# Kernel optimization log

Hardware: AMD Instinct MI355X
Metric: run time of the kernel (lower is better)

The kernel has to match this reference:

```python
import jax, jax.numpy as jnp
import numpy as np

N, E, G = 65536, 262144, 2048
DIN, H, F, L, P, TASK = 9, 300, 32, 5, 3, 1
DG = H + F + 1024 + 167  # 1523


def setup_inputs() -> dict:
    key = jax.random.key(0)
    ks = jax.random.split(key, 24)
    s = 0.02
    inp = {
        'x': jax.random.normal(ks[0], (N, DIN), jnp.float32),
        'morgan': jax.random.uniform(ks[1], (G, 1024), jnp.float32),
        'maccs': jax.random.uniform(ks[2], (G, 167), jnp.float32),
        'edge_index': jax.random.randint(ks[3], (2, E), 0, N, jnp.int32),
        'batch': jnp.sort(jax.random.randint(ks[4], (N,), 0, G, jnp.int32)),
        # node feature encoder
        'W_emb': s * jax.random.normal(ks[5], (DIN, H), jnp.float32),
        'b_emb': jnp.zeros((H,), jnp.float32),
        # GIN conv MLPs (L layers): H -> 2H -> H
        'gin_W1': s * jax.random.normal(ks[6], (L, H, 2 * H), jnp.float32),
        'gin_b1': jnp.zeros((L, 2 * H), jnp.float32),
        'gin_W2': s * jax.random.normal(ks[7], (L, 2 * H, H), jnp.float32),
        'gin_b2': jnp.zeros((L, H), jnp.float32),
        'bn_scale': jnp.ones((L, H), jnp.float32),
        'bn_bias': jnp.zeros((L, H), jnp.float32),
        'eps': jnp.zeros((L,), jnp.float32),
        # virtual node: init embedding + update MLPs (L-1 layers)
        'vn0': jnp.zeros((H,), jnp.float32),
        'vn_W1': s * jax.random.normal(ks[8], (L - 1, H, 2 * H), jnp.float32),
        'vn_b1': jnp.zeros((L - 1, 2 * H), jnp.float32),
        'vn_W2': s * jax.random.normal(ks[9], (L - 1, 2 * H, H), jnp.float32),
        'vn_b2': jnp.zeros((L - 1, H), jnp.float32),
        # predictor MLP: DG -> 2H -> TASK
        'Wp1': s * jax.random.normal(ks[10], (DG, 2 * H), jnp.float32),
        'bp1': jnp.zeros((2 * H,), jnp.float32),
        'Wp2': s * jax.random.normal(ks[11], (2 * H, TASK), jnp.float32),
        'bp2': jnp.zeros((TASK,), jnp.float32),
    }
    return inp


def _seg_mean(v, seg, n):
    s = jax.ops.segment_sum(v, seg, num_segments=n)
    c = jax.ops.segment_sum(jnp.ones((v.shape[0], 1), v.dtype), seg, num_segments=n)
    return s / jnp.maximum(c, 1.0)


def _bn(z, scale, bias):
    m = z.mean(0)
    v = z.var(0)
    return (z - m) * jax.lax.rsqrt(v + 1e-5) * scale + bias


def _gnn_and_predict(x, morgan, maccs, W_emb, b_emb, gin_W1, gin_b1, gin_W2, gin_b2,
                     bn_scale, bn_bias, eps, vn0, vn_W1, vn_b1, vn_W2, vn_b2,
                     Wp1, bp1, Wp2, bp2, edge_index, batch):
    n = x.shape[0]
    g = morgan.shape[0]
    nl = gin_W1.shape[0]
    src, dst = edge_index[0], edge_index[1]

    # GIN-virtual backbone (eval mode, dropout off). Note: GNN input is the
    # original x (the permuted ids are appended AFTER the GNN), so h is
    # permutation-independent and computed once.
    h = x @ W_emb + b_emb
    vn = jnp.broadcast_to(vn0, (g, vn0.shape[0]))
    for l in range(nl):
        hv = h + vn[batch]                                       # [N,H]
        agg = jax.ops.segment_sum(hv[src], dst, num_segments=n)  # neighbor sum
        z = (1.0 + eps[l]) * hv + agg
        z = jax.nn.relu(z @ gin_W1[l] + gin_b1[l]) @ gin_W2[l] + gin_b2[l]
        z = _bn(z, bn_scale[l], bn_bias[l])
        if l < nl - 1:
            z = jax.nn.relu(z)
        h = h + z  # residual
        if l < nl - 1:  # virtual node update
            vt = jax.ops.segment_sum(hv, batch, num_segments=g) + vn
            vn = vn + jax.nn.relu(jax.nn.relu(vt @ vn_W1[l] + vn_b1[l]) @ vn_W2[l] + vn_b2[l])

    pooled_h = _seg_mean(h, batch, g)  # [G,H]

    # Segmented random permutation of tiled eye(F) ids, averaged over P perms.
    # Each node gets one_hot(perm_rank_within_graph % F); rank computed by a
    # single lexsort over (batch, random) instead of a per-graph Python loop.
    counts = jax.ops.segment_sum(jnp.ones((n,), jnp.int32), batch, num_segments=g)
    starts = jnp.concatenate([jnp.zeros((1,), jnp.int32),
                              jnp.cumsum(counts)[:-1].astype(jnp.int32)])
    pkey = jax.random.key(42)
    acc = jnp.zeros((g, F), h.dtype)
    for p in range(P):
        r = jax.random.uniform(jax.random.fold_in(pkey, p), (n,))
        order = jnp.lexsort((r, batch))                       # sort by graph, then random
        local = jnp.arange(n, dtype=jnp.int32) - starts[batch[order]]
        rank = jnp.zeros((n,), jnp.int32).at[order].set(local)  # random rank in graph
        ids = jax.nn.one_hot(rank % F, F, dtype=h.dtype)        # [N,F]
        acc = acc + _seg_mean(ids, batch, g)
    id_pool = acc / P

    # h_rep order matches torch: [pooled h | pooled ids | morgan | maccs]
    h_rep = jnp.concatenate([pooled_h, id_pool, morgan, maccs], axis=1)  # [G,1523]
    return jax.nn.relu(h_rep @ Wp1 + bp1) @ Wp2 + bp2  # [G,TASK]


def reference(x, morgan, maccs, W_emb, b_emb, gin_W1, gin_b1, gin_W2, gin_b2,
              bn_scale, bn_bias, eps, vn0, vn_W1, vn_b1, vn_W2, vn_b2,
              Wp1, bp1, Wp2, bp2, edge_index, batch):
    return _gnn_and_predict(x, morgan, maccs, W_emb, b_emb, gin_W1, gin_b1,
                            gin_W2, gin_b2, bn_scale, bn_bias, eps, vn0,
                            vn_W1, vn_b1, vn_W2, vn_b2, Wp1, bp1, Wp2, bp2,
                            edge_index, batch)
```

## Files before the change

kernel.cpp:

```cpp
#include <hip/hip_runtime.h>

typedef unsigned short u16;
typedef unsigned int u32;
typedef __attribute__((ext_vector_type(8))) short bf16x8_t;
typedef __attribute__((ext_vector_type(4))) float f32x4_t;

#define kN 65536
#define kE 262144
#define kG 2048
#define kH 300
#define kH2 600
#define kL 5
#define kF 32
#define kDG 1523
#define KP_H 320
#define KP_H2 640
#define KP_DG 1536
#define NP_H2 640
#define NP_H 320
#define HVS 320
#define HVS32 160

__device__ __forceinline__ float bf2f(u16 x) {
    union { u32 u; float f; } v; v.u = ((u32)x) << 16; return v.f;
}
__device__ __forceinline__ u16 f2bf(float f) {
    union { float f; u32 u; } v; v.f = f;
    u32 u = v.u;
    u32 r = (u + 0x7fffu + ((u >> 16) & 1u)) >> 16;
    return (u16)r;
}
__device__ __forceinline__ float blo(u32 v) { return bf2f((u16)(v & 0xffffu)); }
__device__ __forceinline__ float bhi(u32 v) { return bf2f((u16)(v >> 16)); }
__device__ __forceinline__ u32 pack2(float lo, float hi) {
    return (u32)f2bf(lo) | ((u32)f2bf(hi) << 16);
}

__device__ __forceinline__ void gld16(const u16* g, u16* l) {
    __builtin_amdgcn_global_load_lds(
        (const __attribute__((address_space(1))) u32*)g,
        (__attribute__((address_space(3))) u32*)l, 16, 0, 0);
}

__device__ __forceinline__ void swz_tile(int& m, int& n) {
    int p = blockIdx.x + gridDim.x * blockIdx.y;
    int xcd = p & 7;
    int q = p >> 3;
    int NB = gridDim.y;
    int mb8 = gridDim.x >> 3;
    m = xcd * mb8 + q / NB;
    n = q % NB;
}

__global__ void transpose_k(const float* __restrict__ W, u16* __restrict__ Wt,
                            int K, int NN, int NP, int KP, long total) {
    long idx = (long)blockIdx.x * 256 + threadIdx.x;
    if (idx >= total) return;
    int per = NP * KP;
    int b = (int)(idx / per);
    int r = (int)(idx % per);
    int n = r / KP;
    int k = r % KP;
    u16 v = 0;
    if (n < NN && k < K) v = f2bf(W[(long)b * K * NN + (long)k * NN + n]);
    Wt[idx] = v;
}

__global__ void hist_g_k(const int* __restrict__ batch, int* __restrict__ counts) {
    int n = blockIdx.x * 256 + threadIdx.x;
    if (n < kN) atomicAdd(&counts[batch[n]], 1);
}

__global__ void scan_g_k(const int* __restrict__ counts, int* __restrict__ starts) {
    __shared__ int s[1024];
    int t = threadIdx.x;
    int c0 = counts[2 * t], c1 = counts[2 * t + 1];
    s[t] = c0 + c1;
    __syncthreads();
    for (int off = 1; off < 1024; off <<= 1) {
        int v = (t >= off) ? s[t - off] : 0;
        __syncthreads();
        s[t] += v;
        __syncthreads();
    }
    int excl = (t > 0) ? s[t - 1] : 0;
    starts[2 * t] = excl;
    starts[2 * t + 1] = excl + c0;
}

__global__ void hist_n_k(const int* __restrict__ ei, int* __restrict__ cnt) {
    int e = blockIdx.x * 256 + threadIdx.x;
    if (e < kE) atomicAdd(&cnt[ei[kE + e]], 1);
}

__global__ void scanA_k(const int* __restrict__ cnt, int* __restrict__ start, int* __restrict__ bsum) {
    __shared__ int s[1024];
    int b = blockIdx.x, t = threadIdx.x;
    int v = cnt[b * 1024 + t];
    s[t] = v;
    __syncthreads();
    for (int off = 1; off < 1024; off <<= 1) {
        int u = (t >= off) ? s[t - off] : 0;
        __syncthreads();
        s[t] += u;
        __syncthreads();
    }
    start[b * 1024 + t] = s[t] - v;
    if (t == 1023) bsum[b] = s[1023];
}

__global__ void scanB_k(int* __restrict__ bsum) {
    if (threadIdx.x == 0) {
        int s = 0;
        for (int i = 0; i < kN / 1024; i++) { s += bsum[i]; bsum[i] = s; }
    }
}

__global__ void scanC_k(int* __restrict__ start, const int* __restrict__ bsum) {
    int b = blockIdx.x, t = threadIdx.x;
    int add = (b > 0) ? bsum[b - 1] : 0;
    start[b * 1024 + t] += add;
    if (b == kN / 1024 - 1 && t == 1023) start[kN] = bsum[kN / 1024 - 1];
}

__global__ void fill_n_k(const int* __restrict__ ei, const int* __restrict__ start,
                         int* __restrict__ fill, int* __restrict__ perm) {
    int e = blockIdx.x * 256 + threadIdx.x;
    if (e >= kE) return;
    int s = ei[e], d = ei[kE + e];
    int pos = start[d] + atomicAdd(&fill[d], 1);
    perm[pos] = s;
}

__global__ __launch_bounds__(256) void embed_k(
    const float* __restrict__ x, const float* __restrict__ W,
    const float* __restrict__ b, const float* __restrict__ vn0,
    u32* __restrict__ hv32) {
    __shared__ float sW[9 * kH];
    __shared__ float sBV[kH];
    int tid = threadIdx.x;
    for (int i = tid; i < 9 * kH; i += 256) sW[i] = W[i];
    for (int i = tid; i < kH; i += 256) sBV[i] = b[i] + vn0[i];
    __syncthreads();
    int wave = tid >> 6, lane = tid & 63;
    int n = blockIdx.x * 4 + wave;
    float xv[9];
    #pragma unroll
    for (int d = 0; d < 9; d++) xv[d] = x[n * 9 + d];
    #pragma unroll
    for (int p = 0; p < 3; p++) {
        int ii = lane + p * 64;
        if (ii < 150) {
            int c0 = 2 * ii;
            float a0 = sBV[c0], a1 = sBV[c0 + 1];
            #pragma unroll
            for (int d = 0; d < 9; d++) {
                a0 += xv[d] * sW[d * kH + c0];
                a1 += xv[d] * sW[d * kH + c0 + 1];
            }
            hv32[(long)n * HVS32 + ii] = pack2(a0, a1);
        } else if (ii < HVS32) {
            hv32[(long)n * HVS32 + ii] = 0u;
        }
    }
}

__global__ void vninit_k(const float* __restrict__ vn0, float* __restrict__ vn) {
    int g = blockIdx.x, c = threadIdx.x;
    if (c < kH) vn[g * kH + c] = vn0[c];
}

__global__ __launch_bounds__(256) void gather_combine_k(
    const u32* __restrict__ hv32, const int* __restrict__ start_n,
    const int* __restrict__ perm, const float* __restrict__ eps, int l,
    u32* __restrict__ out32, float* __restrict__ stats) {
    int tid = threadIdx.x;
    int wave = tid >> 6, lane = tid & 63;
    int n = blockIdx.x * 4 + wave;
    int st = start_n[n], en = start_n[n + 1];
    int i0 = lane, i1 = lane + 64, i2 = lane + 128;
    bool p2 = (i2 < 150);
    float a0 = 0.f, b0 = 0.f, a1 = 0.f, b1 = 0.f, a2 = 0.f, b2 = 0.f;
    int e = st;
    for (; e + 4 <= en; e += 4) {
        const u32* rA = hv32 + (long)perm[e] * HVS32;
        const u32* rB = hv32 + (long)perm[e + 1] * HVS32;
        const u32* rC = hv32 + (long)perm[e + 2] * HVS32;
        const u32* rD = hv32 + (long)perm[e + 3] * HVS32;
        u32 vA0 = rA[i0], vA1 = rA[i1], vA2 = p2 ? rA[i2] : 0u;
        u32 vB0 = rB[i0], vB1 = rB[i1], vB2 = p2 ? rB[i2] : 0u;
        u32 vC0 = rC[i0], vC1 = rC[i1], vC2 = p2 ? rC[i2] : 0u;
        u32 vD0 = rD[i0], vD1 = rD[i1], vD2 = p2 ? rD[i2] : 0u;
        a0 += (blo(vA0) + blo(vB0)) + (blo(vC0) + blo(vD0));
        b0 += (bhi(vA0) + bhi(vB0)) + (bhi(vC0) + bhi(vD0));
        a1 += (blo(vA1) + blo(vB1)) + (blo(vC1) + blo(vD1));
        b1 += (bhi(vA1) + bhi(vB1)) + (bhi(vC1) + bhi(vD1));
        a2 += (blo(vA2) + blo(vB2)) + (blo(vC2) + blo(vD2));
        b2 += (bhi(vA2) + bhi(vB2)) + (bhi(vC2) + bhi(vD2));
    }
    for (; e + 2 <= en; e += 2) {
        const u32* rA = hv32 + (long)perm[e] * HVS32;
        const u32* rB = hv32 + (long)perm[e + 1] * HVS32;
        u32 vA0 = rA[i0], vA1 = rA[i1], vA2 = p2 ? rA[i2] : 0u;
        u32 vB0 = rB[i0], vB1 = rB[i1], vB2 = p2 ? rB[i2] : 0u;
        a0 += blo(vA0) + blo(vB0); b0 += bhi(vA0) + bhi(vB0);
        a1 += blo(vA1) + blo(vB1); b1 += bhi(vA1) + bhi(vB1);
        a2 += blo(vA2) + blo(vB2); b2 += bhi(vA2) + bhi(vB2);
    }
    if (e < en) {
        const u32* rA = hv32 + (long)perm[e] * HVS32;
        u32 vA0 = rA[i0], vA1 = rA[i1], vA2 = p2 ? rA[i2] : 0u;
        a0 += blo(vA0); b0 += bhi(vA0);
        a1 += blo(vA1); b1 += bhi(vA1);
        a2 += blo(vA2); b2 += bhi(vA2);
    }
    const u32* self = hv32 + (long)n * HVS32;
    float ep = 1.f + eps[l];
    u32 s0 = self[i0], s1 = self[i1];
    u32* o = out32 + (long)n * HVS32;
    o[i0] = pack2(ep * blo(s0) + a0, ep * bhi(s0) + b0);
    o[i1] = pack2(ep * blo(s1) + a1, ep * bhi(s1) + b1);
    if (p2) {
        u32 s2 = self[i2];
        o[i2] = pack2(ep * blo(s2) + a2, ep * bhi(s2) + b2);
    } else if (i2 < HVS32) {
        o[i2] = 0u;
    }
    int gz = blockIdx.x * 256 + tid;
    if (gz < 2 * kH) stats[gz] = 0.f;
}

__global__ __launch_bounds__(256) void vt_fin_k(
    const u32* __restrict__ hv32, const float* __restrict__ vncur,
    const int* __restrict__ counts, const int* __restrict__ starts,
    u32* __restrict__ vt32) {
    int tid = threadIdx.x, wave = tid >> 6, lane = tid & 63;
    int g = blockIdx.x * 4 + wave;
    int cnt = counts[g], st = starts[g];
    int i0 = lane, i1 = lane + 64, i2 = lane + 128;
    bool p2 = (i2 < 150);
    float a0 = 0.f, b0 = 0.f, a1 = 0.f, b1 = 0.f, a2 = 0.f, b2 = 0.f;
    int i = 0;
    for (; i + 4 <= cnt; i += 4) {
        const u32* rA = hv32 + (long)(st + i) * HVS32;
        const u32* rB = hv32 + (long)(st + i + 1) * HVS32;
        const u32* rC = hv32 + (long)(st + i + 2) * HVS32;
        const u32* rD = hv32 + (long)(st + i + 3) * HVS32;
        u32 vA0 = rA[i0], vA1 = rA[i1], vA2 = p2 ? rA[i2] : 0u;
        u32 vB0 = rB[i0], vB1 = rB[i1], vB2 = p2 ? rB[i2] : 0u;
        u32 vC0 = rC[i0], vC1 = rC[i1], vC2 = p2 ? rC[i2] : 0u;
        u32 vD0 = rD[i0], vD1 = rD[i1], vD2 = p2 ? rD[i2] : 0u;
        a0 += (blo(vA0) + blo(vB0)) + (blo(vC0) + blo(vD0));
        b0 += (bhi(vA0) + bhi(vB0)) + (bhi(vC0) + bhi(vD0));
        a1 += (blo(vA1) + blo(vB1)) + (blo(vC1) + blo(vD1));
        b1 += (bhi(vA1) + bhi(vB1)) + (bhi(vC1) + bhi(vD1));
        a2 += (blo(vA2) + blo(vB2)) + (blo(vC2) + blo(vD2));
        b2 += (bhi(vA2) + bhi(vB2)) + (bhi(vC2) + bhi(vD2));
    }
    for (; i < cnt; i++) {
        const u32* rA = hv32 + (long)(st + i) * HVS32;
        u32 vA0 = rA[i0], vA1 = rA[i1], vA2 = p2 ? rA[i2] : 0u;
        a0 += blo(vA0); b0 += bhi(vA0);
        a1 += blo(vA1); b1 += bhi(vA1);
        a2 += blo(vA2); b2 += bhi(vA2);
    }
    const float* vg = vncur + g * kH;
    vt32[(long)g * HVS32 + i0] = pack2(a0 + vg[2 * i0], b0 + vg[2 * i0 + 1]);
    vt32[(long)g * HVS32 + i1] = pack2(a1 + vg[2 * i1], b1 + vg[2 * i1 + 1]);
    if (p2) vt32[(long)g * HVS32 + i2] = pack2(a2 + vg[2 * i2], b2 + vg[2 * i2 + 1]);
    else if (i2 < HVS32) vt32[(long)g * HVS32 + i2] = 0u;
}

template<int ACT, int OUT_BF16, int BN_STATS>
__global__ __launch_bounds__(256) void gemm_k(
    const u16* __restrict__ A, const u16* __restrict__ Wt,
    const float* __restrict__ bias, void* __restrict__ out,
    float* __restrict__ stats,
    int KP, int NN, int out_stride, int store_cols) {
    __shared__ __align__(16) u16 lA[128 * 64];
    __shared__ __align__(16) u16 lB[128 * 64];
    __shared__ float sred[128][2];

    const int tid = threadIdx.x;
    const int lane = tid & 63;
    const int wave = tid >> 6;
    const int l16 = lane & 15;
    const int quad = lane >> 4;
    const int wm = (wave & 1) * 64;
    const int wn = (wave >> 1) * 64;
    int sm, sn;
    swz_tile(sm, sn);
    const long tm = (long)sm * 128;
    const int tn = sn * 128;

    const int srow = lane >> 3;
    const int sch = (lane & 7) ^ srow;

    f32x4_t acc[4][4];
    #pragma unroll
    for (int i = 0; i < 4; i++)
        #pragma unroll
        for (int j = 0; j < 4; j++) acc[i][j] = (f32x4_t){0.f, 0.f, 0.f, 0.f};

    for (int k0 = 0; k0 < KP; k0 += 64) {
        __syncthreads();
        #pragma unroll
        for (int j = 0; j < 4; j++) {
            int rb = wave * 32 + j * 8;
            int r = rb + srow;
            gld16(A + (tm + r) * KP + k0 + sch * 8, &lA[rb * 64]);
            gld16(Wt + (long)(tn + r) * KP + k0 + sch * 8, &lB[rb * 64]);
        }
        __syncthreads();
        #pragma unroll
        for (int ks = 0; ks < 2; ks++) {
            bf16x8_t af[4], bfr[4];
            #pragma unroll
            for (int mt = 0; mt < 4; mt++) {
                int row = wm + mt * 16 + l16;
                int phys = (ks * 4 + quad) ^ (l16 & 7);
                af[mt] = *(const bf16x8_t*)&lA[row * 64 + phys * 8];
            }
            #pragma unroll
            for (int nt = 0; nt < 4; nt++) {
                int row = wn + nt * 16 + l16;
                int phys = (ks * 4 + quad) ^ (l16 & 7);
                bfr[nt] = *(const bf16x8_t*)&lB[row * 64 + phys * 8];
            }
            #pragma unroll
            for (int mt = 0; mt < 4; mt++)
                #pragma unroll
                for (int nt = 0; nt < 4; nt++)
                    acc[mt][nt] = __builtin_amdgcn_mfma_f32_16x16x32_bf16(af[mt], bfr[nt], acc[mt][nt], 0, 0, 0);
        }
    }

    if (BN_STATS) {
        if (tid < 128) { sred[tid][0] = 0.f; sred[tid][1] = 0.f; }
    }
    __syncthreads();

    #pragma unroll
    for (int nt = 0; nt < 4; nt++) {
        int col = tn + wn + nt * 16 + l16;
        float bv = (col < NN) ? bias[col] : 0.f;
        float s = 0.f, s2 = 0.f;
        #pragma unroll
        for (int mt = 0; mt < 4; mt++) {
            #pragma unroll
            for (int r = 0; r < 4; r++) {
                long row = tm + wm + mt * 16 + quad * 4 + r;
                float v = acc[mt][nt][r] + bv;
                if (ACT) v = fmaxf(v, 0.f);
                float sv = (col < NN) ? v : 0.f;
                if (col < store_cols) {
                    if (OUT_BF16) ((u16*)out)[row * out_stride + col] = f2bf(sv);
                    else          ((float*)out)[row * out_stride + col] = sv;
                }
                s += sv; s2 += sv * sv;
            }
        }
        if (BN_STATS) {
            atomicAdd(&sred[wn + nt * 16 + l16][0], s);
            atomicAdd(&sred[wn + nt * 16 + l16][1], s2);
        }
    }
    if (BN_STATS) {
        __syncthreads();
        if (tid < 128) {
            int col = tn + tid;
            if (col < NN) {
                atomicAdd(&stats[col], sred[tid][0]);
                atomicAdd(&stats[NN + col], sred[tid][1]);
            }
        }
    }
}

template<int ACT, int OUT_MODE, int BN_STATS>
__global__ __launch_bounds__(256) void gemm64_k(
    const u16* __restrict__ A, const u16* __restrict__ Wt,
    const float* __restrict__ bias, void* __restrict__ out,
    float* __restrict__ stats, const float* __restrict__ vnacc,
    int KP, int NN, int out_stride, int store_cols) {
    __shared__ __align__(16) u16 lA[2][128 * 64];
    __shared__ __align__(16) u16 lB[2][64 * 64];
    __shared__ float sred[64][2];

    const int tid = threadIdx.x;
    const int lane = tid & 63;
    const int wave = tid >> 6;
    const int l16 = lane & 15;
    const int quad = lane >> 4;
    const int wm = (wave & 1) * 64;
    const int wn = (wave >> 1) * 32;
    int sm, sn;
    swz_tile(sm, sn);
    const long tm = (long)sm * 128;
    const int tn = sn * 64;

    const int srow = lane >> 3;
    const int sch = (lane & 7) ^ srow;

    f32x4_t acc[4][2];
    #pragma unroll
    for (int i = 0; i < 4; i++)
        #pragma unroll
        for (int j = 0; j < 2; j++) acc[i][j] = (f32x4_t){0.f, 0.f, 0.f, 0.f};

    auto stage = [&](int bb, int k0) {
        #pragma unroll
        for (int j = 0; j < 4; j++) {
            int rb = wave * 32 + j * 8;
            gld16(A + (tm + rb + srow) * KP + k0 + sch * 8, &lA[bb][rb * 64]);
        }
        #pragma unroll
        for (int j = 0; j < 2; j++) {
            int rb = wave * 16 + j * 8;
            gld16(Wt + (long)(tn + rb + srow) * KP + k0 + sch * 8, &lB[bb][rb * 64]);
        }
    };

    const int nk = KP >> 6;
    stage(0, 0);
    __syncthreads();
    int cur = 0;
    for (int t = 0; t < nk; t++) {
        if (t + 1 < nk) stage(cur ^ 1, (t + 1) << 6);
        #pragma unroll
        for (int ks = 0; ks < 2; ks++) {
            bf16x8_t af[4], bfr[2];
            #pragma unroll
            for (int mt = 0; mt < 4; mt++) {
                int row = wm + mt * 16 + l16;
                int phys = (ks * 4 + quad) ^ (l16 & 7);
                af[mt] = *(const bf16x8_t*)&lA[cur][row * 64 + phys * 8];
            }
            #pragma unroll
            for (int nt = 0; nt < 2; nt++) {
                int row = wn + nt * 16 + l16;
                int phys = (ks * 4 + quad) ^ (l16 & 7);
                bfr[nt] = *(const bf16x8_t*)&lB[cur][row * 64 + phys * 8];
            }
            #pragma unroll
            for (int mt = 0; mt < 4; mt++)
                #pragma unroll
                for (int nt = 0; nt < 2; nt++)
                    acc[mt][nt] = __builtin_amdgcn_mfma_f32_16x16x32_bf16(af[mt], bfr[nt], acc[mt][nt], 0, 0, 0);
        }
        __syncthreads();
        cur ^= 1;
    }

    if (BN_STATS) {
        if (tid < 64) { sred[tid][0] = 0.f; sred[tid][1] = 0.f; }
    }
    __syncthreads();

    #pragma unroll
    for (int nt = 0; nt < 2; nt++) {
        int col = tn + wn + nt * 16 + l16;
        float bv = (col < NN) ? bias[col] : 0.f;
        float s = 0.f, s2 = 0.f;
        #pragma unroll
        for (int mt = 0; mt < 4; mt++) {
            #pragma unroll
            for (int r = 0; r < 4; r++) {
                long row = tm + wm + mt * 16 + quad * 4 + r;
                float v = acc[mt][nt][r] + bv;
                if (ACT) v = fmaxf(v, 0.f);
                float sv = (col < NN) ? v : 0.f;
                if (col < store_cols) {
                    if (OUT_MODE == 1) ((u16*)out)[row * out_stride + col] = f2bf(sv);
                    else if (OUT_MODE == 2)
                        ((float*)out)[row * out_stride + col] =
                            vnacc[row * out_stride + col] + fmaxf(v, 0.f);
                    else ((float*)out)[row * out_stride + col] = sv;
                }
                s += sv; s2 += sv * sv;
            }
        }
        if (BN_STATS) {
            atomicAdd(&sred[wn + nt * 16 + l16][0], s);
            atomicAdd(&sred[wn + nt * 16 + l16][1], s2);
        }
    }
    if (BN_STATS) {
        __syncthreads();
        if (tid < 64) {
            int col = tn + tid;
            if (col < NN) {
                atomicAdd(&stats[col], sred[tid][0]);
                atomicAdd(&stats[NN + col], sred[tid][1]);
            }
        }
    }
}

template<int RELU>
__global__ __launch_bounds__(256) void resid_k(
    u32* __restrict__ hvb32, const u32* __restrict__ z32,
    const float* __restrict__ stats,
    const float* __restrict__ scale, const float* __restrict__ bias, int l,
    const int* __restrict__ batch,
    const float* __restrict__ vncur, const float* __restrict__ vnnxt) {
    int tid = threadIdx.x;
    int wave = tid >> 6, lane = tid & 63;
    int n = blockIdx.x * 4 + wave;
    int g = batch[n];
    #pragma unroll
    for (int p = 0; p < 3; p++) {
        int ii = lane + p * 64;
        if (ii >= 150) break;
        int c0 = 2 * ii;
        float m0 = stats[c0] * (1.f / (float)kN), m1 = stats[c0 + 1] * (1.f / (float)kN);
        float v0 = fmaxf(stats[kH + c0] * (1.f / (float)kN) - m0 * m0, 0.f);
        float v1 = fmaxf(stats[kH + c0 + 1] * (1.f / (float)kN) - m1 * m1, 0.f);
        float a0 = scale[l * kH + c0] * rsqrtf(v0 + 1e-5f);
        float a1 = scale[l * kH + c0 + 1] * rsqrtf(v1 + 1e-5f);
        float d0 = bias[l * kH + c0] - m0 * a0;
        float d1 = bias[l * kH + c0 + 1] - m1 * a1;
        u32 zz = z32[(long)n * HVS32 + ii];
        u32 ho = hvb32[(long)n * HVS32 + ii];
        float2 vc = *(const float2*)(vncur + g * kH + c0);
        float2 vx = *(const float2*)(vnnxt + g * kH + c0);
        float t0 = blo(zz) * a0 + d0;
        float t1 = bhi(zz) * a1 + d1;
        if (RELU) { t0 = fmaxf(t0, 0.f); t1 = fmaxf(t1, 0.f); }
        float h0 = (blo(ho) - vc.x) + t0;
        float h1 = (bhi(ho) - vc.y) + t1;
        hvb32[(long)n * HVS32 + ii] = pack2(h0 + vx.x, h1 + vx.y);
    }
}

__global__ __launch_bounds__(256) void pooled_k(
    const u32* __restrict__ hv32, const float* __restrict__ vnlast,
    const int* __restrict__ counts, const int* __restrict__ starts,
    u32* __restrict__ hrep32) {
    int tid = threadIdx.x, wave = tid >> 6, lane = tid & 63;
    int g = blockIdx.x * 4 + wave;
    int cnt = counts[g], st = starts[g];
    int i0 = lane, i1 = lane + 64, i2 = lane + 128;
    bool p2 = (i2 < 150);
    float a0 = 0.f, b0 = 0.f, a1 = 0.f, b1 = 0.f, a2 = 0.f, b2 = 0.f;
    int i = 0;
    for (; i + 4 <= cnt; i += 4) {
        const u32* rA = hv32 + (long)(st + i) * HVS32;
        const u32* rB = hv32 + (long)(st + i + 1) * HVS32;
        const u32* rC = hv32 + (long)(st + i + 2) * HVS32;
        const u32* rD = hv32 + (long)(st + i + 3) * HVS32;
        u32 vA0 = rA[i0], vA1 = rA[i1], vA2 = p2 ? rA[i2] : 0u;
        u32 vB0 = rB[i0], vB1 = rB[i1], vB2 = p2 ? rB[i2] : 0u;
        u32 vC0 = rC[i0], vC1 = rC[i1], vC2 = p2 ? rC[i2] : 0u;
        u32 vD0 = rD[i0], vD1 = rD[i1], vD2 = p2 ? rD[i2] : 0u;
        a0 += (blo(vA0) + blo(vB0)) + (blo(vC0) + blo(vD0));
        b0 += (bhi(vA0) + bhi(vB0)) + (bhi(vC0) + bhi(vD0));
        a1 += (blo(vA1) + blo(vB1)) + (blo(vC1) + blo(vD1));
        b1 += (bhi(vA1) + bhi(vB1)) + (bhi(vC1) + bhi(vD1));
        a2 += (blo(vA2) + blo(vB2)) + (blo(vC2) + blo(vD2));
        b2 += (bhi(vA2) + bhi(vB2)) + (bhi(vC2) + bhi(vD2));
    }
    for (; i < cnt; i++) {
        const u32* rA = hv32 + (long)(st + i) * HVS32;
        u32 vA0 = rA[i0], vA1 = rA[i1], vA2 = p2 ? rA[i2] : 0u;
        a0 += blo(vA0); b0 += bhi(vA0);
        a1 += blo(vA1); b1 += bhi(vA1);
        a2 += blo(vA2); b2 += bhi(vA2);
    }
    float fc = (float)cnt;
    float inv = 1.f / (float)(cnt > 0 ? cnt : 1);
    const float* vg = vnlast + g * kH;
    hrep32[(long)g * 768 + i0] = pack2((a0 - fc * vg[2 * i0]) * inv, (b0 - fc * vg[2 * i0 + 1]) * inv);
    hrep32[(long)g * 768 + i1] = pack2((a1 - fc * vg[2 * i1]) * inv, (b1 - fc * vg[2 * i1 + 1]) * inv);
    if (p2)
        hrep32[(long)g * 768 + i2] = pack2((a2 - fc * vg[2 * i2]) * inv, (b2 - fc * vg[2 * i2 + 1]) * inv);
}

__global__ void hrep_rest_k(const float* __restrict__ morgan, const float* __restrict__ maccs,
                            const int* __restrict__ counts, u16* __restrict__ hrep) {
    long idx = (long)blockIdx.x * 256 + threadIdx.x;
    if (idx >= (long)kG * (KP_DG - kH)) return;
    int g = (int)(idx / (KP_DG - kH));
    int j = (int)(idx % (KP_DG - kH));
    int col = kH + j;
    u16 v;
    if (j < kF) {
        int c = counts[g];
        int q = (j < c) ? ((c - 1 - j) / kF + 1) : 0;
        v = f2bf((float)q / (float)(c > 0 ? c : 1));
    } else if (j < kF + 1024) {
        v = f2bf(morgan[(long)g * 1024 + (j - kF)]);
    } else if (j < kF + 1024 + 167) {
        v = f2bf(maccs[(long)g * 167 + (j - kF - 1024)]);
    } else {
        v = 0;
    }
    hrep[(long)g * KP_DG + col] = v;
}

__global__ void final_k(const u16* __restrict__ zp, const float* __restrict__ Wp2,
                        const float* __restrict__ bp2, float* __restrict__ out) {
    int wave = threadIdx.x >> 6, lane = threadIdx.x & 63;
    int g = blockIdx.x * 4 + wave;
    float acc = 0.f;
    for (int c = lane; c < kH2; c += 64) acc += bf2f(zp[(long)g * KP_H2 + c]) * Wp2[c];
    #pragma unroll
    for (int off = 32; off; off >>= 1) acc += __shfl_down(acc, off);
    if (lane == 0) out[g] = acc + bp2[0];
}

extern "C" void kernel_launch(void* const* d_in, const int* in_sizes, int n_in,
                              void* d_out, int out_size, void* d_ws, size_t ws_size,
                              hipStream_t stream) {
    const float* x      = (const float*)d_in[0];
    const float* morgan = (const float*)d_in[1];
    const float* maccs  = (const float*)d_in[2];
    const int*   ei     = (const int*)d_in[3];
    const int*   batch  = (const int*)d_in[4];
    const float* W_emb  = (const float*)d_in[5];
    const float* b_emb  = (const float*)d_in[6];
    const float* gin_W1 = (const float*)d_in[7];
    const float* gin_b1 = (const float*)d_in[8];
    const float* gin_W2 = (const float*)d_in[9];
    const float* gin_b2 = (const float*)d_in[10];
    const float* bn_scale = (const float*)d_in[11];
    const float* bn_bias  = (const float*)d_in[12];
    const float* eps    = (const float*)d_in[13];
    const float* vn0    = (const float*)d_in[14];
    const float* vn_W1  = (const float*)d_in[15];
    const float* vn_b1  = (const float*)d_in[16];
    const float* vn_W2  = (const float*)d_in[17];
    const float* vn_b2  = (const float*)d_in[18];
    const float* Wp1    = (const float*)d_in[19];
    const float* bp1    = (const float*)d_in[20];
    const float* Wp2    = (const float*)d_in[21];
    const float* bp2    = (const float*)d_in[22];
    float* out = (float*)d_out;

    char* ws = (char*)d_ws;
    size_t off = 0;
    auto alloc = [&](size_t bytes) -> char* {
        char* p = ws + off;
        off += (bytes + 255) & ~(size_t)255;
        return p;
    };
    u16*   hvbf = (u16*)alloc((size_t)kN * HVS * 2);
    u16*   hv   = (u16*)alloc((size_t)kN * KP_H * 2);
    u16*   z1   = (u16*)alloc((size_t)kN * KP_H2 * 2);
    float* vnA  = (float*)alloc((size_t)kG * kH * 4);
    float* vnB  = (float*)alloc((size_t)kG * kH * 4);
    int* counts = (int*)alloc(kG * 4);
    int* starts = (int*)alloc(kG * 4);
    float* stats = (float*)alloc(2 * kH * 4);
    int* cnt_n  = (int*)alloc((size_t)kN * 4);
    int* start_n = (int*)alloc((size_t)(kN + 1) * 4);
    int* fill_n = (int*)alloc((size_t)kN * 4);
    int* bsum   = (int*)alloc((kN / 1024) * 4);
    int* perm   = (int*)alloc((size_t)kE * 4);
    u16* Wt_g1 = (u16*)alloc((size_t)kL * NP_H2 * KP_H * 2);
    u16* Wt_g2 = (u16*)alloc((size_t)kL * NP_H * KP_H2 * 2);
    u16* Wt_v1 = (u16*)alloc((size_t)(kL - 1) * NP_H2 * KP_H * 2);
    u16* Wt_v2 = (u16*)alloc((size_t)(kL - 1) * NP_H * KP_H2 * 2);
    u16* Wt_p1 = (u16*)alloc((size_t)NP_H2 * KP_DG * 2);
    if (off > ws_size) return;

    u16* vt_in = z1;
    u16* z1v   = z1 + (size_t)4 * 1024 * 1024;
    u16* hrep  = z1;
    u16* zp    = z1 + (size_t)8 * 1024 * 1024;
    float* vnb[2] = {vnA, vnB};

    {
        long t1 = (long)kL * NP_H2 * KP_H;
        transpose_k<<<dim3((unsigned)((t1 + 255) / 256)), 256, 0, stream>>>(gin_W1, Wt_g1, kH, kH2, NP_H2, KP_H, t1);
        long t2 = (long)kL * NP_H * KP_H2;
        transpose_k<<<dim3((unsigned)((t2 + 255) / 256)), 256, 0, stream>>>(gin_W2, Wt_g2, kH2, kH, NP_H, KP_H2, t2);
        long t3 = (long)(kL - 1) * NP_H2 * KP_H;
        transpose_k<<<dim3((unsigned)((t3 + 255) / 256)), 256, 0, stream>>>(vn_W1, Wt_v1, kH, kH2, NP_H2, KP_H, t3);
        long t4 = (long)(kL - 1) * NP_H * KP_H2;
        transpose_k<<<dim3((unsigned)((t4 + 255) / 256)), 256, 0, stream>>>(vn_W2, Wt_v2, kH2, kH, NP_H, KP_H2, t4);
        long t5 = (long)NP_H2 * KP_DG;
        transpose_k<<<dim3((unsigned)((t5 + 255) / 256)), 256, 0, stream>>>(Wp1, Wt_p1, kDG, kH2, NP_H2, KP_DG, t5);
    }

    hipMemsetAsync(counts, 0, kG * 4, stream);
    hipMemsetAsync(cnt_n, 0, (size_t)kN * 4, stream);
    hipMemsetAsync(fill_n, 0, (size_t)kN * 4, stream);
    hist_g_k<<<kN / 256, 256, 0, stream>>>(batch, counts);
    scan_g_k<<<1, 1024, 0, stream>>>(counts, starts);
    hist_n_k<<<kE / 256, 256, 0, stream>>>(ei, cnt_n);
    scanA_k<<<kN / 1024, 1024, 0, stream>>>(cnt_n, start_n, bsum);
    scanB_k<<<1, 64, 0, stream>>>(bsum);
    scanC_k<<<kN / 1024, 1024, 0, stream>>>(start_n, bsum);
    fill_n_k<<<kE / 256, 256, 0, stream>>>(ei, start_n, fill_n, perm);

    embed_k<<<kN / 4, 256, 0, stream>>>(x, W_emb, b_emb, vn0, (u32*)hvbf);
    vninit_k<<<kG, 320, 0, stream>>>(vn0, vnA);

    for (int l = 0; l < kL; l++) {
        float* vcur = vnb[l & 1];
        float* vnxt = vnb[(l + 1) & 1];
        gather_combine_k<<<kN / 4, 256, 0, stream>>>(
            (const u32*)hvbf, start_n, perm, eps, l, (u32*)hv, stats);
        if (l < kL - 1) {
            vt_fin_k<<<kG / 4, 256, 0, stream>>>(
                (const u32*)hvbf, vcur, counts, starts, (u32*)vt_in);
            gemm_k<1, 1, 0><<<dim3(16, NP_H2 / 128), 256, 0, stream>>>(
                vt_in, Wt_v1 + (size_t)l * NP_H2 * KP_H, vn_b1 + l * kH2,
                z1v, nullptr, KP_H, kH2, KP_H2, KP_H2);
            gemm64_k<0, 2, 0><<<dim3(16, NP_H / 64), 256, 0, stream>>>(
                z1v, Wt_v2 + (size_t)l * NP_H * KP_H2, vn_b2 + l * kH,
                vnxt, nullptr, vcur, KP_H2, kH, kH, kH);
        }
        gemm_k<1, 1, 0><<<dim3(kN / 128, NP_H2 / 128), 256, 0, stream>>>(
            hv, Wt_g1 + (size_t)l * NP_H2 * KP_H, gin_b1 + l * kH2,
            z1, nullptr, KP_H, kH2, KP_H2, KP_H2);
        gemm64_k<0, 1, 1><<<dim3(kN / 128, NP_H / 64), 256, 0, stream>>>(
            z1, Wt_g2 + (size_t)l * NP_H * KP_H2, gin_b2 + l * kH,
            hv, stats, nullptr, KP_H2, kH, KP_H, KP_H);
        if (l < kL - 1)
            resid_k<1><<<kN / 4, 256, 0, stream>>>(
                (u32*)hvbf, (const u32*)hv, stats, bn_scale, bn_bias, l, batch, vcur, vnxt);
        else
            resid_k<0><<<kN / 4, 256, 0, stream>>>(
                (u32*)hvbf, (const u32*)hv, stats, bn_scale, bn_bias, l, batch, vcur, vcur);
    }

    float* vnlast = vnb[(kL - 1) & 1];
    pooled_k<<<kG / 4, 256, 0, stream>>>(
        (const u32*)hvbf, vnlast, counts, starts, (u32*)hrep);
    {
        long tr = (long)kG * (KP_DG - kH);
        hrep_rest_k<<<dim3((unsigned)((tr + 255) / 256)), 256, 0, stream>>>(morgan, maccs, counts, hrep);
    }
    gemm_k<1, 1, 0><<<dim3(16, NP_H2 / 128), 256, 0, stream>>>(
        hrep, Wt_p1, bp1, zp, nullptr, KP_DG, kH2, KP_H2, KP_H2);
    final_k<<<kG / 4, 256, 0, stream>>>(zp, Wp2, bp2, out);
}
```

Measured before the change: 1.321 ms.

## Double-buffer GEMM LDS tiles with two-stage prefetch and explicit vmcnt waits

After: 1.323 ms. Within noise of the previous version (+0.2%).

```diff
diff --git a/kernel.cpp b/kernel.cpp
--- a/kernel.cpp
+++ b/kernel.cpp
@@ -40,6 +40,15 @@
     __builtin_amdgcn_global_load_lds(
         (const __attribute__((address_space(1))) u32*)g,
         (__attribute__((address_space(3))) u32*)l, 16, 0, 0);
+}
+
+__device__ __forceinline__ void vwait6() { asm volatile("s_waitcnt vmcnt(6)" ::: "memory"); }
+__device__ __forceinline__ void vwait8() { asm volatile("s_waitcnt vmcnt(8)" ::: "memory"); }
+__device__ __forceinline__ void vwait0() { asm volatile("s_waitcnt vmcnt(0)" ::: "memory"); }
+__device__ __forceinline__ void rbar() {
+    __builtin_amdgcn_sched_barrier(0);
+    __builtin_amdgcn_s_barrier();
+    __builtin_amdgcn_sched_barrier(0);
 }
 
 __device__ __forceinline__ void swz_tile(int& m, int& n) {
@@ -277,8 +286,8 @@
     const float* __restrict__ bias, void* __restrict__ out,
     float* __restrict__ stats,
     int KP, int NN, int out_stride, int store_cols) {
-    __shared__ __align__(16) u16 lA[128 * 64];
-    __shared__ __align__(16) u16 lB[128 * 64];
+    __shared__ __align__(16) u16 lA[2][128 * 64];
+    __shared__ __align__(16) u16 lB[2][128 * 64];
     __shared__ float sred[128][2];
 
     const int tid = threadIdx.x;
@@ -302,16 +311,24 @@
         #pragma unroll
         for (int j = 0; j < 4; j++) acc[i][j] = (f32x4_t){0.f, 0.f, 0.f, 0.f};
 
-    for (int k0 = 0; k0 < KP; k0 += 64) {
-        __syncthreads();
+    auto stage = [&](int bb, int k0) {
         #pragma unroll
         for (int j = 0; j < 4; j++) {
             int rb = wave * 32 + j * 8;
             int r = rb + srow;
-            gld16(A + (tm + r) * KP + k0 + sch * 8, &lA[rb * 64]);
-            gld16(Wt + (long)(tn + r) * KP + k0 + sch * 8, &lB[rb * 64]);
-        }
-        __syncthreads();
+            gld16(A + (tm + r) * KP + k0 + sch * 8, &lA[bb][rb * 64]);
+            gld16(Wt + (long)(tn + r) * KP + k0 + sch * 8, &lB[bb][rb * 64]);
+        }
+    };
+
+    const int nk = KP >> 6;
+    stage(0, 0);
+    if (nk > 1) stage(1, 64);
+    for (int t = 0; t < nk; t++) {
+        if (t < nk - 1) vwait8(); else vwait0();
+        rbar();
+        const u16* la = lA[t & 1];
+        const u16* lb = lB[t & 1];
         #pragma unroll
         for (int ks = 0; ks < 2; ks++) {
             bf16x8_t af[4], bfr[4];
@@ -319,13 +336,13 @@
             for (int mt = 0; mt < 4; mt++) {
                 int row = wm + mt * 16 + l16;
                 int phys = (ks * 4 + quad) ^ (l16 & 7);
-                af[mt] = *(const bf16x8_t*)&lA[row * 64 + phys * 8];
+                af[mt] = *(const bf16x8_t*)&la[row * 64 + phys * 8];
             }
             #pragma unroll
             for (int nt = 0; nt < 4; nt++) {
                 int row = wn + nt * 16 + l16;
                 int phys = (ks * 4 + quad) ^ (l16 & 7);
-                bfr[nt] = *(const bf16x8_t*)&lB[row * 64 + phys * 8];
+                bfr[nt] = *(const bf16x8_t*)&lb[row * 64 + phys * 8];
             }
             #pragma unroll
             for (int mt = 0; mt < 4; mt++)
@@ -333,6 +350,8 @@
                 for (int nt = 0; nt < 4; nt++)
                     acc[mt][nt] = __builtin_amdgcn_mfma_f32_16x16x32_bf16(af[mt], bfr[nt], acc[mt][nt], 0, 0, 0);
         }
+        rbar();
+        if (t + 2 < nk) stage(t & 1, (t + 2) * 64);
     }
 
     if (BN_STATS) {
@@ -423,10 +442,12 @@
 
     const int nk = KP >> 6;
     stage(0, 0);
-    __syncthreads();
-    int cur = 0;
+    if (nk > 1) stage(1, 64);
     for (int t = 0; t < nk; t++) {
-        if (t + 1 < nk) stage(cur ^ 1, (t + 1) << 6);
+        if (t < nk - 1) vwait6(); else vwait0();
+        rbar();
+        const u16* la = lA[t & 1];
+        const u16* lb = lB[t & 1];
         #pragma unroll
         for (int ks = 0; ks < 2; ks++) {
             bf16x8_t af[4], bfr[2];
@@ -434,13 +455,13 @@
             for (int mt = 0; mt < 4; mt++) {
                 int row = wm + mt * 16 + l16;
                 int phys = (ks * 4 + quad) ^ (l16 & 7);
-                af[mt] = *(const bf16x8_t*)&lA[cur][row * 64 + phys * 8];
+                af[mt] = *(const bf16x8_t*)&la[row * 64 + phys * 8];
             }
             #pragma unroll
             for (int nt = 0; nt < 2; nt++) {
                 int row = wn + nt * 16 + l16;
                 int phys = (ks * 4 + quad) ^ (l16 & 7);
-                bfr[nt] = *(const bf16x8_t*)&lB[cur][row * 64 + phys * 8];
+                bfr[nt] = *(const bf16x8_t*)&lb[row * 64 + phys * 8];
             }
             #pragma unroll
             for (int mt = 0; mt < 4; mt++)
@@ -448,8 +469,8 @@
                 for (int nt = 0; nt < 2; nt++)
                     acc[mt][nt] = __builtin_amdgcn_mfma_f32_16x16x32_bf16(af[mt], bfr[nt], acc[mt][nt], 0, 0, 0);
         }
-        __syncthreads();
-        cur ^= 1;
+        rbar();
+        if (t + 2 < nk) stage(t & 1, (t + 2) * 64);
     }
 
     if (BN_STATS) {
```
